# Kernel optimization log

Hardware: AMD Instinct MI355X
Metric: run time of the kernel (lower is better)

Reference implementation:

```python
import jax, jax.numpy as jnp
import numpy as np
import math

DIM = 2048
H = 16
KV = 4
HD = DIM // H  # 128
ROPE_DIM = 64  # head_dim * rope_fraction(0.5), even
ROPE_BASE = 10000.0
EPS_RMS = 1.1920928955078125e-07  # torch fp32 finfo eps (F.rms_norm default)


def rms_norm(t):
    # F.rms_norm over last dim, no weight
    return t * jax.lax.rsqrt(jnp.mean(t * t, axis=-1, keepdims=True) + EPS_RMS)


def rope_tables(seqlen, dtype):
    inv_freq = 1.0 / (ROPE_BASE ** (jnp.arange(0, ROPE_DIM, 2, dtype=jnp.float32) / ROPE_DIM))
    t = jnp.arange(seqlen, dtype=jnp.float32)
    freqs = jnp.outer(t, inv_freq)  # [S, ROPE_DIM//2]
    return jnp.cos(freqs).astype(dtype)[None, None], jnp.sin(freqs).astype(dtype)[None, None]


def apply_partial_rope(x, cos, sin):
    # x: [B, h, S, HD]; rotate first ROPE_DIM dims, pass through the rest
    xr = x[..., :ROPE_DIM]
    half = ROPE_DIM // 2
    x1, x2 = xr[..., :half], xr[..., half:]
    rotated = jnp.concatenate((x1 * cos + x2 * sin, -x1 * sin + x2 * cos), axis=-1)
    return jnp.concatenate((rotated, x[..., ROPE_DIM:]), axis=-1)


def setup_inputs() -> dict:
    key = jax.random.key(0)
    ks = jax.random.split(key, 5)
    B, S = 4, 1024
    x = jax.random.normal(ks[0], (B, S, DIM), dtype=jnp.float32)
    Wq = jax.random.normal(ks[1], (DIM, DIM), dtype=jnp.float32) * 0.02
    Wk = jax.random.normal(ks[2], (KV * HD, DIM), dtype=jnp.float32) * 0.02
    Wv = jax.random.normal(ks[3], (KV * HD, DIM), dtype=jnp.float32) * 0.02
    Wproj = jax.random.normal(ks[4], (DIM, DIM), dtype=jnp.float32) * 0.02
    # causal boolean mask [B, S, S]
    causal = jnp.tril(jnp.ones((S, S), dtype=bool))
    attn_mask = jnp.broadcast_to(causal[None], (B, S, S))
    return {"x": x, "attn_mask": attn_mask, "Wq": Wq, "Wk": Wk, "Wv": Wv, "Wproj": Wproj}


def reference(x, attn_mask, Wq, Wk, Wv, Wproj):
    B, S, D = x.shape
    repeat = H // KV
    q = (x @ Wq.T).reshape(B, S, H, HD).transpose(0, 2, 1, 3)   # [B,H,S,HD]
    k = (x @ Wk.T).reshape(B, S, KV, HD).transpose(0, 2, 1, 3)  # [B,KV,S,HD]
    v = (x @ Wv.T).reshape(B, S, KV, HD).transpose(0, 2, 1, 3)
    q = rms_norm(q)
    k = rms_norm(k)
    cos, sin = rope_tables(S, q.dtype)
    q = apply_partial_rope(q, cos, sin)
    k = apply_partial_rope(k, cos, sin)
    # GQA: expand kv heads
    k_rep = jnp.repeat(k, repeat, axis=1)  # [B,H,S,HD]
    v_rep = jnp.repeat(v, repeat, axis=1)
    bias = jnp.where(attn_mask[:, None], jnp.float32(0.0), jnp.float32(-10000.0)).astype(q.dtype)
    scores = jnp.einsum('bhqd,bhkd->bhqk', q, k_rep) / math.sqrt(HD) + bias
    attn = jax.nn.softmax(scores, axis=-1)
    y = jnp.einsum('bhqk,bhkd->bhqd', attn, v_rep)
    valid = jnp.any(attn_mask, axis=-1)[:, None, :, None].astype(y.dtype)
    y = y * valid
    # xsa: remove component of y along self value vector
    denom = jnp.maximum(jnp.sum(v_rep * v_rep, axis=-1, keepdims=True), 1e-06)
    proj = jnp.sum(y * v_rep, axis=-1, keepdims=True) / denom
    y = y - proj * v_rep
    y = y.transpose(0, 2, 1, 3).reshape(B, S, D)
    return y @ Wproj.T
```

## Files before the change

kernel.cpp:

```cpp
#include <hip/hip_runtime.h>


typedef __attribute__((ext_vector_type(8))) __bf16 bf16x8;
typedef __attribute__((ext_vector_type(4))) __bf16 bf16x4;
typedef __attribute__((ext_vector_type(4))) float f32x4;

static_assert(sizeof(__bf16) == 2, "bf16 size");

#define MFMA16x16x32(a, b, c) __builtin_amdgcn_mfma_f32_16x16x32_bf16((a), (b), (c), 0, 0, 0)

#if __has_builtin(__builtin_amdgcn_exp2f)
#define EXP2(x) __builtin_amdgcn_exp2f(x)
#else
#define EXP2(x) exp2f(x)
#endif

__device__ __forceinline__ void gload_lds16(const void* g, void* l) {
  __builtin_amdgcn_global_load_lds((const __attribute__((address_space(1))) void*)g,
                                   (__attribute__((address_space(3))) void*)l, 16, 0, 0);
}

__global__ __launch_bounds__(256) void cast_f2b(const float* __restrict__ in,
                                                __bf16* __restrict__ out, int n4) {
  int i = blockIdx.x * blockDim.x + threadIdx.x;
  const int stride = gridDim.x * blockDim.x;
  for (; i < n4; i += stride) {
    f32x4 v = ((const f32x4*)in)[i];
    bf16x4 o;
    o[0] = (__bf16)v[0];
    o[1] = (__bf16)v[1];
    o[2] = (__bf16)v[2];
    o[3] = (__bf16)v[3];
    ((bf16x4*)out)[i] = o;
  }
}

__global__ __launch_bounds__(256) void cast3_f2b(const float* __restrict__ wq,
                                                 const float* __restrict__ wk,
                                                 const float* __restrict__ wv,
                                                 __bf16* __restrict__ out) {
  const int n1 = 2048 * 2048 / 4, n2 = 512 * 2048 / 4;
  const int ntot = n1 + 2 * n2;
  int i = blockIdx.x * blockDim.x + threadIdx.x;
  const int stride = gridDim.x * blockDim.x;
  for (; i < ntot; i += stride) {
    const float* src;
    int j = i;
    if (j < n1) {
      src = wq;
    } else if (j < n1 + n2) {
      src = wk;
      j -= n1;
    } else {
      src = wv;
      j -= n1 + n2;
    }
    f32x4 v = ((const f32x4*)src)[j];
    bf16x4 o;
    o[0] = (__bf16)v[0];
    o[1] = (__bf16)v[1];
    o[2] = (__bf16)v[2];
    o[3] = (__bf16)v[3];
    ((bf16x4*)out)[i] = o;
  }
}

template <typename CT>
__global__ __launch_bounds__(256) void gemm_bt(const __bf16* __restrict__ A,
                                               const __bf16* __restrict__ B,
                                               CT* __restrict__ C, int M, int N, int K,
                                               int nbn) {
  __shared__ __bf16 As[2][128 * 32];
  __shared__ __bf16 Bs[2][128 * 32];
  const int nwg = gridDim.x;
  const int id = blockIdx.x;
  const int xid = (id & 7) * (nwg >> 3) + (id >> 3);
  const int bm = xid / nbn;
  const int bn = xid - bm * nbn;
  const int t = threadIdx.x;
  const int l = t & 63, w = t >> 6;
  const int wr = w >> 1, wc = w & 1;
  const int lr = l & 15, lk = l >> 4;
  const __bf16* Ab = A + (size_t)bm * 128 * K;
  const __bf16* Bb = B + (size_t)bn * 128 * K;
  const int srow = t >> 2;
  const int scol = ((t & 3) ^ ((srow >> 1) & 3)) << 3;
  f32x4 acc[4][4] = {};

  auto stage = [&](int k0, int buf) {
    gload_lds16(Ab + (size_t)srow * K + k0 + scol, &As[buf][t * 8]);
    gload_lds16(Ab + (size_t)(srow + 64) * K + k0 + scol, &As[buf][2048 + t * 8]);
    gload_lds16(Bb + (size_t)srow * K + k0 + scol, &Bs[buf][t * 8]);
    gload_lds16(Bb + (size_t)(srow + 64) * K + k0 + scol, &Bs[buf][2048 + t * 8]);
  };

  stage(0, 0);
  __syncthreads();

  const int NT = K >> 5;
  for (int kt = 0; kt < NT; ++kt) {
    const int cur = kt & 1;
    if (kt + 1 < NT) stage((kt + 1) << 5, cur ^ 1);

    bf16x8 af[4], bfr[4];
#pragma unroll
    for (int m = 0; m < 4; ++m) {
      const int row = wr * 64 + m * 16 + lr;
      af[m] = *(const bf16x8*)&As[cur][row * 32 + ((lk ^ ((row >> 1) & 3)) << 3)];
    }
#pragma unroll
    for (int n = 0; n < 4; ++n) {
      const int row = wc * 64 + n * 16 + lr;
      bfr[n] = *(const bf16x8*)&Bs[cur][row * 32 + ((lk ^ ((row >> 1) & 3)) << 3)];
    }
#pragma unroll
    for (int m = 0; m < 4; ++m)
#pragma unroll
      for (int n = 0; n < 4; ++n) acc[m][n] = MFMA16x16x32(af[m], bfr[n], acc[m][n]);

    __syncthreads();
  }

#pragma unroll
  for (int m = 0; m < 4; ++m) {
    const int row0 = bm * 128 + wr * 64 + m * 16 + lk * 4;
#pragma unroll
    for (int n = 0; n < 4; ++n) {
      const int col = bn * 128 + wc * 64 + n * 16 + lr;
#pragma unroll
      for (int i = 0; i < 4; ++i) C[(size_t)(row0 + i) * N + col] = (CT)acc[m][n][i];
    }
  }
}

__global__ __launch_bounds__(256) void normrope(__bf16* __restrict__ qkv) {
  const int w = threadIdx.x >> 6, l = threadIdx.x & 63;
  const int idx = blockIdx.x * 4 + w;
  int m, col0;
  bool isq;
  if (idx < 65536) {
    m = idx >> 4;
    col0 = (idx & 15) << 7;
    isq = true;
  } else {
    const int j = idx - 65536;
    m = j >> 2;
    col0 = 2048 + ((j & 3) << 7);
    isq = false;
  }
  const int s = m & 1023;
  __bf16* p = qkv + (size_t)m * 3072 + col0;
  float v0 = (float)p[l];
  float v1 = (float)p[l + 64];
  float ss = v0 * v0 + v1 * v1;
#pragma unroll
  for (int off = 1; off < 64; off <<= 1) ss += __shfl_xor(ss, off);
  float sc = rsqrtf(ss * (1.0f / 128.0f) + 1.1920928955078125e-07f);
  v0 *= sc;
  v1 *= sc;
  const float other = __shfl_xor(v0, 32);
  const int j = l & 31;
  const float ang = (float)s * powf(10000.0f, -(float)j * 0.03125f);
  const float cs = cosf(ang), sn = sinf(ang);
  float r0;
  if (l < 32)
    r0 = v0 * cs + other * sn;
  else
    r0 = -other * sn + v0 * cs;
  if (isq) {
    const float qs = 0.1275174457f;
    r0 *= qs;
    v1 *= qs;
  }
  p[l] = (__bf16)r0;
  p[l + 64] = (__bf16)v1;
}

__global__ __launch_bounds__(256) void vtrans(const __bf16* __restrict__ qkv,
                                              __bf16* __restrict__ vt) {
  __shared__ __bf16 L[64 * 128];
  const int tile = blockIdx.x;
  const int st = tile & 15, bk = tile >> 4;
  const int b = bk >> 2, kvh = bk & 3;
  const int t = threadIdx.x;
  const int s0 = st * 64;
  const __bf16* src = qkv + ((size_t)(b * 1024 + s0)) * 3072 + 2560 + kvh * 128;
#pragma unroll
  for (int r = 0; r < 4; ++r) {
    const int off = r * 2048 + t * 8;
    const int s = off >> 7, d = off & 127;
    bf16x8 v = *(const bf16x8*)(src + (size_t)s * 3072 + d);
    *(bf16x8*)&L[s * 128 + (d ^ ((s & 7) << 3) ^ (((s >> 3) & 7) << 3))] = v;
  }
  __syncthreads();
  __bf16* dst = vt + (size_t)bk * 128 * 1024;
#pragma unroll
  for (int r = 0; r < 4; ++r) {
    const int off = r * 2048 + t * 8;
    const int d = off >> 6, sc = off & 63;
    bf16x8 v;
#pragma unroll
    for (int j = 0; j < 8; ++j) {
      const int s = sc + j;
      v[j] = L[s * 128 + (d ^ ((s & 7) << 3) ^ (((s >> 3) & 7) << 3))];
    }
    *(bf16x8*)&dst[(size_t)d * 1024 + ((s0 + sc) ^ ((d & 7) << 3))] = v;
  }
}

__global__ __launch_bounds__(512) void attn_fwd(const __bf16* __restrict__ qkv,
                                                const __bf16* __restrict__ vt,
                                                __bf16* __restrict__ y) {
  const int id = blockIdx.x;
  const int g = (id & 7) | (((id >> 3) & 1) << 3);
  const int b = g >> 2, kvh = g & 3;
  const int hi = (id >> 4) & 3;
  const int pr = (id >> 6) & 3;
  const int h = kvh * 4 + hi;

  const int t = threadIdx.x;
  const int l = t & 63, w = t >> 6;
  const int lr = l & 15, lk = l >> 4;
  const int lr8 = lr & 7;

  __shared__ __bf16 Ks[2][64 * 128];
  __shared__ __bf16 Vs[2][128 * 64];
  __shared__ __bf16 Ps[8][16 * 64];

  const size_t rb = (size_t)b * 1024;
  const __bf16* Kg0 = qkv + rb * 3072 + 2048 + kvh * 128;
  const __bf16* Vtb = vt + (size_t)(b * 4 + kvh) * 128 * 1024;

  const int koff0 = t * 8;
  const int krow0 = koff0 >> 7;
  const int kcol0 = (koff0 & 127) ^ ((krow0 & 7) << 3);
  const int koff1 = 4096 + t * 8;
  const int krow1 = koff1 >> 7;
  const int kcol1 = (koff1 & 127) ^ ((krow1 & 7) << 3);
  const int voff0 = t * 8, voff1 = 4096 + t * 8;

#pragma unroll 1
  for (int pass = 0; pass < 2; ++pass) {
    const int qt = pass ? (7 - pr) : pr;
    const int q0 = qt << 7;

    bf16x8 aq[4];
    {
      const __bf16* qrow = qkv + (rb + q0 + w * 16 + lr) * 3072 + h * 128 + lk * 8;
#pragma unroll
      for (int kk = 0; kk < 4; ++kk) aq[kk] = *(const bf16x8*)(qrow + kk * 32);
    }

    float m_i[4], l_i[4];
    f32x4 o[8] = {};
#pragma unroll
    for (int i = 0; i < 4; ++i) {
      m_i[i] = -1e30f;
      l_i[i] = 0.0f;
    }

    const int rowg0 = q0 + w * 16 + lk * 4;
    const int wmin = q0 + w * 16;
    const int wmax = wmin + 15;
    const int nt = 2 * qt + 2;

    gload_lds16(Kg0 + (size_t)krow0 * 3072 + kcol0, &Ks[0][0] + koff0);
    gload_lds16(Kg0 + (size_t)krow1 * 3072 + kcol1, &Ks[0][0] + koff1);
    gload_lds16(Vtb + (size_t)(voff0 >> 6) * 1024 + (voff0 & 63), &Vs[0][0] + voff0);
    gload_lds16(Vtb + (size_t)(voff1 >> 6) * 1024 + (voff1 & 63), &Vs[0][0] + voff1);
    __syncthreads();

    for (int tt = 0; tt < nt; ++tt) {
      const int kv0 = tt * 64;
      const int cur = tt & 1;
      if (tt + 1 < nt) {
        const int nkv = kv0 + 64;
        const __bf16* Kg = Kg0 + (size_t)nkv * 3072;
        __bf16* kd = &Ks[cur ^ 1][0];
        __bf16* vd = &Vs[cur ^ 1][0];
        gload_lds16(Kg + (size_t)krow0 * 3072 + kcol0, kd + koff0);
        gload_lds16(Kg + (size_t)krow1 * 3072 + kcol1, kd + koff1);
        gload_lds16(Vtb + (size_t)(voff0 >> 6) * 1024 + nkv + (voff0 & 63), vd + voff0);
        gload_lds16(Vtb + (size_t)(voff1 >> 6) * 1024 + nkv + (voff1 & 63), vd + voff1);
      }

      if (kv0 <= wmax) {
        f32x4 sacc[4] = {};
#pragma unroll
        for (int kk = 0; kk < 4; ++kk) {
#pragma unroll
          for (int n = 0; n < 4; ++n) {
            const bf16x8 bk = *(const bf16x8*)&Ks[cur][(n * 16 + lr) * 128 +
                                                      ((kk * 32 + lk * 8) ^ (lr8 << 3))];
            sacc[n] = MFMA16x16x32(aq[kk], bk, sacc[n]);
          }
        }

        float pm[4];
#pragma unroll
        for (int i = 0; i < 4; ++i) pm[i] = -1e30f;
        if (kv0 + 63 > wmin) {
#pragma unroll
          for (int n = 0; n < 4; ++n) {
            const int colg = kv0 + n * 16 + lr;
#pragma unroll
            for (int i = 0; i < 4; ++i) {
              if (colg > rowg0 + i) sacc[n][i] = -1e30f;
              pm[i] = fmaxf(pm[i], sacc[n][i]);
            }
          }
        } else {
#pragma unroll
          for (int n = 0; n < 4; ++n)
#pragma unroll
            for (int i = 0; i < 4; ++i) pm[i] = fmaxf(pm[i], sacc[n][i]);
        }
#pragma unroll
        for (int i = 0; i < 4; ++i) {
          pm[i] = fmaxf(pm[i], __shfl_xor(pm[i], 1));
          pm[i] = fmaxf(pm[i], __shfl_xor(pm[i], 2));
          pm[i] = fmaxf(pm[i], __shfl_xor(pm[i], 4));
          pm[i] = fmaxf(pm[i], __shfl_xor(pm[i], 8));
        }
        float alpha[4], rs[4];
#pragma unroll
        for (int i = 0; i < 4; ++i) {
          const float mn = fmaxf(m_i[i], pm[i]);
          alpha[i] = EXP2(m_i[i] - mn);
          m_i[i] = mn;
          rs[i] = 0.0f;
        }
#pragma unroll
        for (int n = 0; n < 4; ++n) {
#pragma unroll
          for (int i = 0; i < 4; ++i) {
            const float p = EXP2(sacc[n][i] - m_i[i]);
            rs[i] += p;
            const int prow = lk * 4 + i;
            Ps[w][prow * 64 + ((n * 16 + lr) ^ ((prow & 7) << 3))] = (__bf16)p;
          }
        }
#pragma unroll
        for (int i = 0; i < 4; ++i) {
          rs[i] += __shfl_xor(rs[i], 1);
          rs[i] += __shfl_xor(rs[i], 2);
          rs[i] += __shfl_xor(rs[i], 4);
          rs[i] += __shfl_xor(rs[i], 8);
          l_i[i] = l_i[i] * alpha[i] + rs[i];
        }
#pragma unroll
        for (int f = 0; f < 8; ++f)
#pragma unroll
          for (int i = 0; i < 4; ++i) o[f][i] *= alpha[i];

#pragma unroll
        for (int ks = 0; ks < 2; ++ks) {
          const bf16x8 pa =
              *(const bf16x8*)&Ps[w][lr * 64 + ((ks * 32 + lk * 8) ^ (lr8 << 3))];
#pragma unroll
          for (int f = 0; f < 8; ++f) {
            const bf16x8 vb = *(const bf16x8*)&Vs[cur][(f * 16 + lr) * 64 +
                                                       ((ks * 32 + lk * 8) ^ (lr8 << 3))];
            o[f] = MFMA16x16x32(pa, vb, o[f]);
          }
        }
      }

      __syncthreads();
    }

#pragma unroll
    for (int i = 0; i < 4; ++i) {
      const int sg = rowg0 + i;
      const size_t mg = rb + sg;
      const __bf16* vp = qkv + mg * 3072 + 2560 + kvh * 128;
      const float invl = 1.0f / l_i[i];
      float vvv[8], yvv[8];
      float dyv = 0.0f, dvv = 0.0f;
#pragma unroll
      for (int f = 0; f < 8; ++f) {
        const float vf = (float)vp[f * 16 + lr];
        const float yf = o[f][i] * invl;
        vvv[f] = vf;
        yvv[f] = yf;
        dyv += yf * vf;
        dvv += vf * vf;
      }
#pragma unroll
      for (int off = 1; off < 16; off <<= 1) {
        dyv += __shfl_xor(dyv, off);
        dvv += __shfl_xor(dvv, off);
      }
      const float proj = dyv / fmaxf(dvv, 1e-6f);
      __bf16* yp = y + mg * 2048 + h * 128;
#pragma unroll
      for (int f = 0; f < 8; ++f) yp[f * 16 + lr] = (__bf16)(yvv[f] - proj * vvv[f]);
    }
  }
}

extern "C" void kernel_launch(void* const* d_in, const int* in_sizes, int n_in,
                              void* d_out, int out_size, void* d_ws, size_t ws_size,
                              hipStream_t stream) {
  const float* x = (const float*)d_in[0];
  const float* Wq = (const float*)d_in[2];
  const float* Wk = (const float*)d_in[3];
  const float* Wv = (const float*)d_in[4];
  const float* Wp = (const float*)d_in[5];
  float* out = (float*)d_out;

  __bf16* xb = (__bf16*)d_ws;
  __bf16* Wb = xb + (size_t)4096 * 2048;
  __bf16* Wpb = Wb + (size_t)3072 * 2048;
  __bf16* qkv = Wpb + (size_t)2048 * 2048;
  __bf16* yb = qkv + (size_t)4096 * 3072;
  __bf16* vt = xb;

  cast_f2b<<<1024, 256, 0, stream>>>(x, xb, 4096 * 2048 / 4);
  cast3_f2b<<<768, 256, 0, stream>>>(Wq, Wk, Wv, Wb);
  cast_f2b<<<512, 256, 0, stream>>>(Wp, Wpb, 2048 * 2048 / 4);

  gemm_bt<__bf16><<<768, 256, 0, stream>>>(xb, Wb, qkv, 4096, 3072, 2048, 24);
  normrope<<<20480, 256, 0, stream>>>(qkv);
  vtrans<<<256, 256, 0, stream>>>(qkv, vt);
  attn_fwd<<<256, 512, 0, stream>>>(qkv, vt, yb);
  gemm_bt<float><<<512, 256, 0, stream>>>(yb, Wpb, out, 4096, 2048, 2048, 16);
}
```

Before: 211.1 us.

## Replace 128x128 GEMM with 256-row, 512-thread tiles and deeper K step

Replaces the 128x128x32 bf16 GEMM with a templated kernel that uses 256xBN tiles, K-step 64, 8 waves per block, an XOR swizzle over 8 column groups, and MFMA priority hints with explicit barrier/waitcnt placement. The larger tile is meant to cut global/LDS traffic per FLOP and improve MFMA density for both the QKV and output projections. In exchange LDS use grows to 128KB for BN=256, the grid shrinks to 192/256 blocks (under one wave across 256 CUs for QKV), and register pressure rises.

```diff
diff --git a/kernel.cpp b/kernel.cpp
--- a/kernel.cpp
+++ b/kernel.cpp
@@ -65,68 +65,89 @@
   }
 }
 
-template <typename CT>
-__global__ __launch_bounds__(256) void gemm_bt(const __bf16* __restrict__ A,
+template <int BN, typename CT>
+__global__ __launch_bounds__(512) void gemm256(const __bf16* __restrict__ A,
                                                const __bf16* __restrict__ B,
-                                               CT* __restrict__ C, int M, int N, int K,
+                                               CT* __restrict__ C, int N, int K,
                                                int nbn) {
-  __shared__ __bf16 As[2][128 * 32];
-  __shared__ __bf16 Bs[2][128 * 32];
+  constexpr int NR = BN / 64;
+  __shared__ __bf16 As[2][256 * 64];
+  __shared__ __bf16 Bs[2][BN * 64];
+
   const int nwg = gridDim.x;
   const int id = blockIdx.x;
   const int xid = (id & 7) * (nwg >> 3) + (id >> 3);
   const int bm = xid / nbn;
   const int bn = xid - bm * nbn;
+
   const int t = threadIdx.x;
   const int l = t & 63, w = t >> 6;
-  const int wr = w >> 1, wc = w & 1;
+  const int wr = w >> 2, wc = w & 3;
   const int lr = l & 15, lk = l >> 4;
-  const __bf16* Ab = A + (size_t)bm * 128 * K;
-  const __bf16* Bb = B + (size_t)bn * 128 * K;
-  const int srow = t >> 2;
-  const int scol = ((t & 3) ^ ((srow >> 1) & 3)) << 3;
-  f32x4 acc[4][4] = {};
-
-  auto stage = [&](int k0, int buf) {
-    gload_lds16(Ab + (size_t)srow * K + k0 + scol, &As[buf][t * 8]);
-    gload_lds16(Ab + (size_t)(srow + 64) * K + k0 + scol, &As[buf][2048 + t * 8]);
-    gload_lds16(Bb + (size_t)srow * K + k0 + scol, &Bs[buf][t * 8]);
-    gload_lds16(Bb + (size_t)(srow + 64) * K + k0 + scol, &Bs[buf][2048 + t * 8]);
+  const __bf16* Ab = A + (size_t)bm * 256 * K;
+  const __bf16* Bb = B + (size_t)bn * BN * K;
+
+  const int srow = t >> 3;
+  const int scol = ((t & 7) ^ (srow & 7)) << 3;
+
+  auto stage = [&](int kt, int buf) {
+    const int k0 = kt << 6;
+#pragma unroll
+    for (int r = 0; r < 4; ++r)
+      gload_lds16(Ab + (size_t)(r * 64 + srow) * K + k0 + scol,
+                  &As[buf][r * 4096 + t * 8]);
+#pragma unroll
+    for (int r = 0; r < BN / 64; ++r)
+      gload_lds16(Bb + (size_t)(r * 64 + srow) * K + k0 + scol,
+                  &Bs[buf][r * 4096 + t * 8]);
   };
+
+  f32x4 acc[8][NR] = {};
 
   stage(0, 0);
   __syncthreads();
 
-  const int NT = K >> 5;
+  const int NT = K >> 6;
   for (int kt = 0; kt < NT; ++kt) {
     const int cur = kt & 1;
-    if (kt + 1 < NT) stage((kt + 1) << 5, cur ^ 1);
-
-    bf16x8 af[4], bfr[4];
-#pragma unroll
-    for (int m = 0; m < 4; ++m) {
-      const int row = wr * 64 + m * 16 + lr;
-      af[m] = *(const bf16x8*)&As[cur][row * 32 + ((lk ^ ((row >> 1) & 3)) << 3)];
-    }
-#pragma unroll
-    for (int n = 0; n < 4; ++n) {
-      const int row = wc * 64 + n * 16 + lr;
-      bfr[n] = *(const bf16x8*)&Bs[cur][row * 32 + ((lk ^ ((row >> 1) & 3)) << 3)];
-    }
-#pragma unroll
-    for (int m = 0; m < 4; ++m)
-#pragma unroll
-      for (int n = 0; n < 4; ++n) acc[m][n] = MFMA16x16x32(af[m], bfr[n], acc[m][n]);
-
-    __syncthreads();
-  }
-
-#pragma unroll
-  for (int m = 0; m < 4; ++m) {
-    const int row0 = bm * 128 + wr * 64 + m * 16 + lk * 4;
-#pragma unroll
-    for (int n = 0; n < 4; ++n) {
-      const int col = bn * 128 + wc * 64 + n * 16 + lr;
+    if (kt + 1 < NT) stage(kt + 1, cur ^ 1);
+
+#pragma unroll
+    for (int kk = 0; kk < 2; ++kk) {
+      bf16x8 af[8], bfr[NR];
+#pragma unroll
+      for (int m = 0; m < 8; ++m) {
+        const int row = wr * 128 + m * 16 + lr;
+        const int cg = (kk * 4 + lk) ^ (row & 7);
+        af[m] = *(const bf16x8*)&As[cur][row * 64 + cg * 8];
+      }
+#pragma unroll
+      for (int n = 0; n < NR; ++n) {
+        const int row = wc * (16 * NR) + n * 16 + lr;
+        const int cg = (kk * 4 + lk) ^ (row & 7);
+        bfr[n] = *(const bf16x8*)&Bs[cur][row * 64 + cg * 8];
+      }
+      __builtin_amdgcn_s_setprio(1);
+#pragma unroll
+      for (int m = 0; m < 8; ++m)
+#pragma unroll
+        for (int n = 0; n < NR; ++n) acc[m][n] = MFMA16x16x32(af[m], bfr[n], acc[m][n]);
+      __builtin_amdgcn_s_setprio(0);
+      if (kk == 0) {
+        __builtin_amdgcn_s_barrier();
+      } else {
+        asm volatile("s_waitcnt vmcnt(0)" ::: "memory");
+        __builtin_amdgcn_s_barrier();
+      }
+    }
+  }
+
+#pragma unroll
+  for (int m = 0; m < 8; ++m) {
+    const int row0 = bm * 256 + wr * 128 + m * 16 + lk * 4;
+#pragma unroll
+    for (int n = 0; n < NR; ++n) {
+      const int col = bn * BN + wc * (16 * NR) + n * 16 + lr;
 #pragma unroll
       for (int i = 0; i < 4; ++i) C[(size_t)(row0 + i) * N + col] = (CT)acc[m][n][i];
     }
@@ -420,9 +441,9 @@
   cast3_f2b<<<768, 256, 0, stream>>>(Wq, Wk, Wv, Wb);
   cast_f2b<<<512, 256, 0, stream>>>(Wp, Wpb, 2048 * 2048 / 4);
 
-  gemm_bt<__bf16><<<768, 256, 0, stream>>>(xb, Wb, qkv, 4096, 3072, 2048, 24);
+  gemm256<256, __bf16><<<192, 512, 0, stream>>>(xb, Wb, qkv, 3072, 2048, 12);
   normrope<<<20480, 256, 0, stream>>>(qkv);
   vtrans<<<256, 256, 0, stream>>>(qkv, vt);
   attn_fwd<<<256, 512, 0, stream>>>(qkv, vt, yb);
-  gemm_bt<float><<<512, 256, 0, stream>>>(yb, Wpb, out, 4096, 2048, 2048, 16);
-}
+  gemm256<128, float><<<256, 512, 0, stream>>>(yb, Wpb, out, 2048, 2048, 16);
+}
```

Measured after the change: 222.3 us. 1.05x slower.

## Fuse RMS-norm and RoPE into QKV GEMM epilogue and merge cast kernels

Applied to the files above, without the earlier changes.

Merges the three fp32-to-bf16 cast kernels into one prep kernel, which also precomputes a cos/sin RoPE table. The QKV GEMM epilogue now does the per-head RMS norm, the rotary embedding and the query scaling, reducing row sums across the two wave columns through shared memory. This removes the separate normrope kernel and its read-modify-write pass over qkv. It also adds s_setprio around the MFMA blocks in attention. In exchange the epilogue gains a sync and strided scalar stores, and the table adds a small extra global read.

```diff
diff --git a/kernel.cpp b/kernel.cpp
--- a/kernel.cpp
+++ b/kernel.cpp
@@ -20,56 +20,59 @@
                                    (__attribute__((address_space(3))) void*)l, 16, 0, 0);
 }
 
-__global__ __launch_bounds__(256) void cast_f2b(const float* __restrict__ in,
-                                                __bf16* __restrict__ out, int n4) {
-  int i = blockIdx.x * blockDim.x + threadIdx.x;
-  const int stride = gridDim.x * blockDim.x;
-  for (; i < n4; i += stride) {
-    f32x4 v = ((const f32x4*)in)[i];
+__global__ __launch_bounds__(256) void prep(const float* __restrict__ x,
+                                            const float* __restrict__ wq,
+                                            const float* __restrict__ wk,
+                                            const float* __restrict__ wv,
+                                            const float* __restrict__ wp,
+                                            __bf16* __restrict__ xb,
+                                            __bf16* __restrict__ wb,
+                                            __bf16* __restrict__ wpb,
+                                            float2* __restrict__ tab) {
+  constexpr int NX = 2097152;
+  constexpr int NW1 = 1048576;
+  constexpr int NW2 = 262144;
+  constexpr int NP = 1048576;
+  constexpr int NT = 32768;
+  constexpr int TOT = NX + NW1 + 2 * NW2 + NP + NT;
+  auto cast4 = [](const float* s, __bf16* d, int i) {
+    f32x4 v = ((const f32x4*)s)[i];
     bf16x4 o;
     o[0] = (__bf16)v[0];
     o[1] = (__bf16)v[1];
     o[2] = (__bf16)v[2];
     o[3] = (__bf16)v[3];
-    ((bf16x4*)out)[i] = o;
-  }
-}
-
-__global__ __launch_bounds__(256) void cast3_f2b(const float* __restrict__ wq,
-                                                 const float* __restrict__ wk,
-                                                 const float* __restrict__ wv,
-                                                 __bf16* __restrict__ out) {
-  const int n1 = 2048 * 2048 / 4, n2 = 512 * 2048 / 4;
-  const int ntot = n1 + 2 * n2;
+    ((bf16x4*)d)[i] = o;
+  };
   int i = blockIdx.x * blockDim.x + threadIdx.x;
   const int stride = gridDim.x * blockDim.x;
-  for (; i < ntot; i += stride) {
-    const float* src;
+  for (; i < TOT; i += stride) {
     int j = i;
-    if (j < n1) {
-      src = wq;
-    } else if (j < n1 + n2) {
-      src = wk;
-      j -= n1;
+    if (j < NX) {
+      cast4(x, xb, j);
+    } else if ((j -= NX) < NW1) {
+      cast4(wq, wb, j);
+    } else if ((j -= NW1) < NW2) {
+      cast4(wk, wb + (size_t)NW1 * 4, j);
+    } else if ((j -= NW2) < NW2) {
+      cast4(wv, wb + (size_t)(NW1 + NW2) * 4, j);
+    } else if ((j -= NW2) < NP) {
+      cast4(wp, wpb, j);
     } else {
-      src = wv;
-      j -= n1 + n2;
-    }
-    f32x4 v = ((const f32x4*)src)[j];
-    bf16x4 o;
-    o[0] = (__bf16)v[0];
-    o[1] = (__bf16)v[1];
-    o[2] = (__bf16)v[2];
-    o[3] = (__bf16)v[3];
-    ((bf16x4*)out)[i] = o;
-  }
-}
-
-template <typename CT>
+      j -= NP;
+      const int s = j >> 5, jj = j & 31;
+      const float inv = powf(10000.0f, -(float)jj * 0.03125f);
+      const float ang = (float)s * inv;
+      tab[j] = make_float2(cosf(ang), sinf(ang));
+    }
+  }
+}
+
+template <typename CT, bool FUSE>
 __global__ __launch_bounds__(256) void gemm_bt(const __bf16* __restrict__ A,
                                                const __bf16* __restrict__ B,
-                                               CT* __restrict__ C, int M, int N, int K,
-                                               int nbn) {
+                                               CT* __restrict__ C, int N, int K, int nbn,
+                                               const float2* __restrict__ tab) {
   __shared__ __bf16 As[2][128 * 32];
   __shared__ __bf16 Bs[2][128 * 32];
   const int nwg = gridDim.x;
@@ -121,6 +124,63 @@
     __syncthreads();
   }
 
+  if constexpr (FUSE) {
+    if (bn < 20) {
+      __shared__ float Ls[2][128];
+      float ssp[4][4];
+#pragma unroll
+      for (int m = 0; m < 4; ++m)
+#pragma unroll
+        for (int i = 0; i < 4; ++i) {
+          float s = 0.0f;
+#pragma unroll
+          for (int n = 0; n < 4; ++n) s += acc[m][n][i] * acc[m][n][i];
+#pragma unroll
+          for (int off = 1; off < 16; off <<= 1) s += __shfl_xor(s, off);
+          ssp[m][i] = s;
+        }
+      if (lr == 0) {
+#pragma unroll
+        for (int m = 0; m < 4; ++m)
+#pragma unroll
+          for (int i = 0; i < 4; ++i)
+            Ls[wc][wr * 64 + m * 16 + lk * 4 + i] = ssp[m][i];
+      }
+      __syncthreads();
+      const bool isq = (bn < 16);
+      const float qs = isq ? 0.1275174457f : 1.0f;
+#pragma unroll
+      for (int m = 0; m < 4; ++m) {
+#pragma unroll
+        for (int i = 0; i < 4; ++i) {
+          const int rl = wr * 64 + m * 16 + lk * 4 + i;
+          const int rg = bm * 128 + rl;
+          const float sc =
+              rsqrtf((Ls[0][rl] + Ls[1][rl]) * (1.0f / 128.0f) +
+                     1.1920928955078125e-07f) *
+              qs;
+          CT* Cr = C + (size_t)rg * N + bn * 128;
+          if (wc == 0) {
+            const int s = rg & 1023;
+#pragma unroll
+            for (int n = 0; n < 2; ++n) {
+              const int j = n * 16 + lr;
+              const float2 cs = tab[s * 32 + j];
+              const float x1 = acc[m][n][i], x2 = acc[m][n + 2][i];
+              Cr[j] = (CT)((x1 * cs.x + x2 * cs.y) * sc);
+              Cr[j + 32] = (CT)((-x1 * cs.y + x2 * cs.x) * sc);
+            }
+          } else {
+#pragma unroll
+            for (int n = 0; n < 4; ++n)
+              Cr[64 + n * 16 + lr] = (CT)(acc[m][n][i] * sc);
+          }
+        }
+      }
+      return;
+    }
+  }
+
 #pragma unroll
   for (int m = 0; m < 4; ++m) {
     const int row0 = bm * 128 + wr * 64 + m * 16 + lk * 4;
@@ -131,49 +191,6 @@
       for (int i = 0; i < 4; ++i) C[(size_t)(row0 + i) * N + col] = (CT)acc[m][n][i];
     }
   }
-}
-
-__global__ __launch_bounds__(256) void normrope(__bf16* __restrict__ qkv) {
-  const int w = threadIdx.x >> 6, l = threadIdx.x & 63;
-  const int idx = blockIdx.x * 4 + w;
-  int m, col0;
-  bool isq;
-  if (idx < 65536) {
-    m = idx >> 4;
-    col0 = (idx & 15) << 7;
-    isq = true;
-  } else {
-    const int j = idx - 65536;
-    m = j >> 2;
-    col0 = 2048 + ((j & 3) << 7);
-    isq = false;
-  }
-  const int s = m & 1023;
-  __bf16* p = qkv + (size_t)m * 3072 + col0;
-  float v0 = (float)p[l];
-  float v1 = (float)p[l + 64];
-  float ss = v0 * v0 + v1 * v1;
-#pragma unroll
-  for (int off = 1; off < 64; off <<= 1) ss += __shfl_xor(ss, off);
-  float sc = rsqrtf(ss * (1.0f / 128.0f) + 1.1920928955078125e-07f);
-  v0 *= sc;
-  v1 *= sc;
-  const float other = __shfl_xor(v0, 32);
-  const int j = l & 31;
-  const float ang = (float)s * powf(10000.0f, -(float)j * 0.03125f);
-  const float cs = cosf(ang), sn = sinf(ang);
-  float r0;
-  if (l < 32)
-    r0 = v0 * cs + other * sn;
-  else
-    r0 = -other * sn + v0 * cs;
-  if (isq) {
-    const float qs = 0.1275174457f;
-    r0 *= qs;
-    v1 *= qs;
-  }
-  p[l] = (__bf16)r0;
-  p[l + 64] = (__bf16)v1;
 }
 
 __global__ __launch_bounds__(256) void vtrans(const __bf16* __restrict__ qkv,
@@ -286,6 +303,7 @@
 
       if (kv0 <= wmax) {
         f32x4 sacc[4] = {};
+        __builtin_amdgcn_s_setprio(1);
 #pragma unroll
         for (int kk = 0; kk < 4; ++kk) {
 #pragma unroll
@@ -295,6 +313,7 @@
             sacc[n] = MFMA16x16x32(aq[kk], bk, sacc[n]);
           }
         }
+        __builtin_amdgcn_s_setprio(0);
 
         float pm[4];
 #pragma unroll
@@ -353,6 +372,7 @@
 #pragma unroll
           for (int i = 0; i < 4; ++i) o[f][i] *= alpha[i];
 
+        __builtin_amdgcn_s_setprio(1);
 #pragma unroll
         for (int ks = 0; ks < 2; ++ks) {
           const bf16x8 pa =
@@ -364,6 +384,7 @@
             o[f] = MFMA16x16x32(pa, vb, o[f]);
           }
         }
+        __builtin_amdgcn_s_setprio(0);
       }
 
       __syncthreads();
@@ -414,15 +435,13 @@
   __bf16* Wpb = Wb + (size_t)3072 * 2048;
   __bf16* qkv = Wpb + (size_t)2048 * 2048;
   __bf16* yb = qkv + (size_t)4096 * 3072;
+  float2* tab = (float2*)(yb + (size_t)4096 * 2048);
   __bf16* vt = xb;
 
-  cast_f2b<<<1024, 256, 0, stream>>>(x, xb, 4096 * 2048 / 4);
-  cast3_f2b<<<768, 256, 0, stream>>>(Wq, Wk, Wv, Wb);
-  cast_f2b<<<512, 256, 0, stream>>>(Wp, Wpb, 2048 * 2048 / 4);
-
-  gemm_bt<__bf16><<<768, 256, 0, stream>>>(xb, Wb, qkv, 4096, 3072, 2048, 24);
-  normrope<<<20480, 256, 0, stream>>>(qkv);
+  prep<<<2048, 256, 0, stream>>>(x, Wq, Wk, Wv, Wp, xb, Wb, Wpb, tab);
+
+  gemm_bt<__bf16, true><<<768, 256, 0, stream>>>(xb, Wb, qkv, 3072, 2048, 24, tab);
   vtrans<<<256, 256, 0, stream>>>(qkv, vt);
   attn_fwd<<<256, 512, 0, stream>>>(qkv, vt, yb);
-  gemm_bt<float><<<512, 256, 0, stream>>>(yb, Wpb, out, 4096, 2048, 2048, 16);
-}
+  gemm_bt<float, false><<<512, 256, 0, stream>>>(yb, Wpb, out, 2048, 2048, 16, nullptr);
+}
```

New measurement: 182.5 us. -13.6%, faster.
